# Optimization experiments

Measured on AMD Instinct MI355X. Metric: run time of the kernel, lower is better.

## Reference

```python
import jax, jax.numpy as jnp
import numpy as np

D_MODEL = 1024
D_MEMORY = 768
NUM_HEADS = 16
HEAD_DIM = D_MODEL // NUM_HEADS


def _linear_params(key, d_in, d_out):
    kw, kb = jax.random.split(key)
    bound = 1.0 / np.sqrt(d_in)
    W = jax.random.uniform(kw, (d_out, d_in), jnp.float32, -bound, bound)
    b = jax.random.uniform(kb, (d_out,), jnp.float32, -bound, bound)
    return W, b


def setup_inputs() -> dict:
    key = jax.random.key(0)
    ks = jax.random.split(key, 9)
    B, S, M = 2, 2048, 4096
    query = jax.random.normal(ks[0], (B, S, D_MODEL), jnp.float32)
    memory_keys = jax.random.normal(ks[1], (B, M, D_MEMORY), jnp.float32)
    memory_values = jax.random.normal(ks[2], (B, M, D_MEMORY), jnp.float32)
    Wq, bq = _linear_params(ks[3], D_MODEL, D_MODEL)
    Wk, bk = _linear_params(ks[4], D_MEMORY, D_MODEL)
    Wv, bv = _linear_params(ks[5], D_MEMORY, D_MODEL)
    Wo, bo = _linear_params(ks[6], D_MODEL, D_MODEL)
    Wg1, bg1 = _linear_params(ks[7], 2 * D_MODEL, D_MODEL)
    Wg2, bg2 = _linear_params(ks[8], D_MODEL, 1)
    return dict(query=query, memory_keys=memory_keys, memory_values=memory_values,
                Wq=Wq, bq=bq, Wk=Wk, bk=bk, Wv=Wv, bv=bv, Wo=Wo, bo=bo,
                Wg1=Wg1, bg1=bg1, Wg2=Wg2, bg2=bg2)


def reference(query, memory_keys, memory_values,
              Wq, bq, Wk, bk, Wv, bv, Wo, bo, Wg1, bg1, Wg2, bg2):
    B, S, _ = query.shape
    M = memory_keys.shape[1]
    H, Dh = NUM_HEADS, HEAD_DIM
    # projections (torch Linear: x @ W.T + b)
    Q = (query @ Wq.T + bq).reshape(B, S, H, Dh)
    K = (memory_keys @ Wk.T + bk).reshape(B, M, H, Dh)
    V = (memory_values @ Wv.T + bv).reshape(B, M, H, Dh)
    scale = Dh ** -0.5
    attn = jnp.einsum('bshd,bmhd->bhsm', Q, K) * scale
    attn = jax.nn.softmax(attn, axis=-1)
    retrieved = jnp.einsum('bhsm,bmhd->bshd', attn, V).reshape(B, S, H * Dh)
    retrieved = retrieved @ Wo.T + bo
    # gate: Linear -> SiLU -> Linear -> Sigmoid on [query; retrieved]
    g = jnp.concatenate([query, retrieved], axis=-1) @ Wg1.T + bg1
    g = jax.nn.silu(g)
    gate = jax.nn.sigmoid(g @ Wg2.T + bg2)  # [B,S,1]
    return query + gate * retrieved
```

## Files before the change

kernel.cpp:

```cpp
#include <hip/hip_runtime.h>

typedef __attribute__((ext_vector_type(8))) __bf16 bf16x8;
typedef __attribute__((ext_vector_type(4))) float f32x4;
typedef __attribute__((ext_vector_type(8))) unsigned short u16x8;

__device__ __forceinline__ ushort f2bf(float x) {
    unsigned u = __builtin_bit_cast(unsigned, x);
    unsigned r = u + 0x7fffu + ((u >> 16) & 1u);
    return (ushort)(r >> 16);
}
__device__ __forceinline__ float bf2f(ushort u) {
    unsigned v = ((unsigned)u) << 16;
    return __builtin_bit_cast(float, v);
}

__device__ __forceinline__ unsigned cvtpk(float lo, float hi) {
    unsigned r;
    asm("v_cvt_pk_bf16_f32 %0, %1, %2" : "=v"(r) : "v"(lo), "v"(hi));
    return r;
}

__device__ __forceinline__ void gload16(const void* g, void* l) {
    __builtin_amdgcn_global_load_lds(
        (const __attribute__((address_space(1))) void*)g,
        (__attribute__((address_space(3))) void*)l,
        16, 0, 0);
}

__global__ __launch_bounds__(256) void cvt_f32_bf16(const float* __restrict__ in,
                                                    ushort* __restrict__ out, int n4) {
    int i = blockIdx.x * 256 + threadIdx.x;
    int stride = gridDim.x * 256;
    for (; i < n4; i += stride) {
        float4 v = ((const float4*)in)[i];
        ushort4 o;
        o.x = f2bf(v.x); o.y = f2bf(v.y); o.z = f2bf(v.z); o.w = f2bf(v.w);
        ((ushort4*)out)[i] = o;
    }
}

__global__ __launch_bounds__(256) void cvt_query_cat(const float* __restrict__ in,
                                                     ushort* __restrict__ cat) {
    const int r = blockIdx.x, t = threadIdx.x;
    float4 v = ((const float4*)(in + (size_t)r * 1024))[t];
    ushort4 o;
    o.x = f2bf(v.x); o.y = f2bf(v.y); o.z = f2bf(v.z); o.w = f2bf(v.w);
    ((ushort4*)(cat + (size_t)r * 2048))[t] = o;
}

template<int EPI>
__global__ __launch_bounds__(256) void gemm_bt(
    const ushort* __restrict__ A, int lda,
    const ushort* __restrict__ Bw, int ldb,
    const float* __restrict__ bias,
    ushort* __restrict__ o_bf, int ld0,
    float* __restrict__ o_f32,
    int K, float scale)
{
    __shared__ __align__(1024) char smem[49152];
    char* As = smem;
    char* Bs = smem + 32768;
    const int t = threadIdx.x, w = t >> 6, l = t & 63, g = l >> 4, c = l & 15;
    const int wr = w >> 1, wc = w & 1;
    const long m0 = (long)blockIdx.y * 128, n0 = (long)blockIdx.x * 64;
    const size_t ldaB = (size_t)lda * 2, ldbB = (size_t)ldb * 2;
    const int swz = (c & 7) << 4;

    f32x4 acc[4][2];
#pragma unroll
    for (int i = 0; i < 4; ++i)
#pragma unroll
        for (int j = 0; j < 2; ++j) acc[i][j] = (f32x4)0.0f;

    auto stage = [&](int kt, int bufsel) {
        const char* Ab = (const char*)A + (size_t)kt * 128;
        const char* Bb = (const char*)Bw + (size_t)kt * 128;
#pragma unroll
        for (int i = 0; i < 4; ++i) {
            int o = (i * 4 + w) * 1024 + l * 16;
            int row = o >> 7, cb = o & 127;
            gload16(Ab + (size_t)(m0 + row) * ldaB + (cb ^ ((row & 7) << 4)),
                    As + bufsel * 16384 + (i * 4 + w) * 1024);
        }
#pragma unroll
        for (int i = 0; i < 2; ++i) {
            int o = (i * 4 + w) * 1024 + l * 16;
            int row = o >> 7, cb = o & 127;
            gload16(Bb + (size_t)(n0 + row) * ldbB + (cb ^ ((row & 7) << 4)),
                    Bs + bufsel * 8192 + (i * 4 + w) * 1024);
        }
    };

    const int nkt = K >> 6;
    stage(0, 0);
    __syncthreads();

    for (int kt = 0; kt < nkt; ++kt) {
        const int cur = kt & 1;
        if (kt + 1 < nkt) stage(kt + 1, cur ^ 1);
        const char* Ac = As + cur * 16384;
        const char* Bc = Bs + cur * 8192;
        bf16x8 af[2][4], bfr[2][2];
#pragma unroll
        for (int kf = 0; kf < 2; ++kf) {
            int cbk = (kf * 64 + g * 16) ^ swz;
#pragma unroll
            for (int i = 0; i < 4; ++i)
                af[kf][i] = *(const bf16x8*)(Ac + (wr * 64 + i * 16 + c) * 128 + cbk);
#pragma unroll
            for (int j = 0; j < 2; ++j)
                bfr[kf][j] = *(const bf16x8*)(Bc + (wc * 32 + j * 16 + c) * 128 + cbk);
        }
#pragma unroll
        for (int kf = 0; kf < 2; ++kf)
#pragma unroll
            for (int i = 0; i < 4; ++i)
#pragma unroll
                for (int j = 0; j < 2; ++j)
                    acc[i][j] = __builtin_amdgcn_mfma_f32_16x16x32_bf16(
                        af[kf][i], bfr[kf][j], acc[i][j], 0, 0, 0);
        __syncthreads();
    }

#pragma unroll
    for (int i = 0; i < 4; ++i)
#pragma unroll
        for (int j = 0; j < 2; ++j) {
            const long col = n0 + wc * 32 + j * 16 + c;
            const float bs = bias[col];
            const long rowb = m0 + wr * 64 + i * 16 + g * 4;
            if (EPI == 1) {
                ushort4 o;
                o.x = f2bf(acc[i][j][0] + bs);
                o.y = f2bf(acc[i][j][1] + bs);
                o.z = f2bf(acc[i][j][2] + bs);
                o.w = f2bf(acc[i][j][3] + bs);
                *(ushort4*)(o_bf + col * (long)ld0 + rowb) = o;
            } else {
#pragma unroll
                for (int jj = 0; jj < 4; ++jj) {
                    const long row = rowb + jj;
                    const float v = acc[i][j][jj] + bs;
                    if (EPI == 0) {
                        o_bf[row * (long)ld0 + col] = f2bf(v * scale);
                    } else if (EPI == 2) {
                        o_f32[row * (long)ld0 + col] = v;
                        o_bf[row * 2048 + col] = f2bf(v);
                    } else {
                        const float sv = v / (1.0f + __expf(-v));
                        o_bf[row * (long)ld0 + col] = f2bf(sv);
                    }
                }
            }
        }
}

__global__ __launch_bounds__(256, 4) void attn_fwd(
    const ushort* __restrict__ qp, const ushort* __restrict__ kp,
    const ushort* __restrict__ vT, ushort* __restrict__ out)
{
    __shared__ __align__(1024) char smem[40960];
    const int t = threadIdx.x, w = t >> 6, l = t & 63, g = l >> 4, c = l & 15;
    const int b = blockIdx.z, h = blockIdx.y;
    const int s0 = blockIdx.x * 64 + w * 16;
    const int swz = (c & 7) << 4;

    const size_t qbase = ((size_t)b * 2048 + s0 + c) * 1024 + h * 64 + g * 8;
    const bf16x8 qf0 = *(const bf16x8*)(qp + qbase);
    const bf16x8 qf1 = *(const bf16x8*)(qp + qbase + 32);

    const u16x8 ones_u = (u16x8)(ushort)0x3F80;
    const bf16x8 ones = __builtin_bit_cast(bf16x8, ones_u);

    f32x4 oacc[4];
    f32x4 lacc = (f32x4)0.0f;
#pragma unroll
    for (int d = 0; d < 4; ++d) oacc[d] = (f32x4)0.0f;
    float mrow = -1e30f;

    const char* kpB = (const char*)kp + (size_t)b * 4096 * 2048 + h * 128;
    const char* vTB = (const char*)vT + (size_t)h * 64 * 16384 + (size_t)b * 4096 * 2;
    char* Pw = smem + 32768 + w * 2048;

    auto stage = [&](int mt, int bufsel) {
#pragma unroll
        for (int i = 0; i < 2; ++i) {
            int o = (i * 4 + w) * 1024 + l * 16;
            int row = o >> 7, cb = o & 127;
            gload16(kpB + (size_t)(mt + row) * 2048 + (cb ^ ((row & 7) << 4)),
                    smem + bufsel * 8192 + (i * 4 + w) * 1024);
            gload16(vTB + (size_t)row * 16384 + (size_t)mt * 2 + (cb ^ ((row & 7) << 4)),
                    smem + 16384 + bufsel * 8192 + (i * 4 + w) * 1024);
        }
    };

    stage(0, 0);
    __syncthreads();

    for (int ti = 0; ti < 64; ++ti) {
        const int cur = ti & 1;
        if (ti < 63) stage((ti + 1) << 6, cur ^ 1);
        const char* Ksc = smem + cur * 8192;
        const char* Vsc = smem + 16384 + cur * 8192;

        f32x4 sacc[4];
#pragma unroll
        for (int mf = 0; mf < 4; ++mf) sacc[mf] = (f32x4)0.0f;
#pragma unroll
        for (int kf = 0; kf < 2; ++kf) {
            const int cbk = (kf * 64 + g * 16) ^ swz;
            const bf16x8 q = kf ? qf1 : qf0;
#pragma unroll
            for (int mf = 0; mf < 4; ++mf) {
                bf16x8 kb = *(const bf16x8*)(Ksc + (mf * 16 + c) * 128 + cbk);
                sacc[mf] = __builtin_amdgcn_mfma_f32_16x16x32_bf16(kb, q, sacc[mf], 0, 0, 0);
            }
        }

        float tm;
        {
            float a0 = fmaxf(fmaxf(sacc[0][0], sacc[0][1]), fmaxf(sacc[0][2], sacc[0][3]));
            float a1 = fmaxf(fmaxf(sacc[1][0], sacc[1][1]), fmaxf(sacc[1][2], sacc[1][3]));
            float a2 = fmaxf(fmaxf(sacc[2][0], sacc[2][1]), fmaxf(sacc[2][2], sacc[2][3]));
            float a3 = fmaxf(fmaxf(sacc[3][0], sacc[3][1]), fmaxf(sacc[3][2], sacc[3][3]));
            tm = fmaxf(fmaxf(a0, a1), fmaxf(a2, a3));
        }
        tm = fmaxf(tm, __shfl_xor(tm, 16));
        tm = fmaxf(tm, __shfl_xor(tm, 32));

        if (!__all(tm <= mrow + 8.0f)) {
            const float nm = fmaxf(mrow, tm);
            const float al = exp2f(mrow - nm);
            mrow = nm;
#pragma unroll
            for (int j = 0; j < 4; ++j) {
                const float alr = __shfl(al, g * 4 + j);
                lacc[j] *= alr;
#pragma unroll
                for (int df = 0; df < 4; ++df) oacc[df][j] *= alr;
            }
        }

        asm volatile("" ::: "memory");
#pragma unroll
        for (int mf = 0; mf < 4; ++mf) {
            const float p0 = exp2f(sacc[mf][0] - mrow);
            const float p1 = exp2f(sacc[mf][1] - mrow);
            const float p2 = exp2f(sacc[mf][2] - mrow);
            const float p3 = exp2f(sacc[mf][3] - mrow);
            const unsigned u0 = cvtpk(p0, p1);
            const unsigned u1 = cvtpk(p2, p3);
            const unsigned long long pw = ((unsigned long long)u1 << 32) | (unsigned long long)u0;
            *(unsigned long long*)(Pw + c * 128 + ((mf * 32 + g * 8) ^ swz)) = pw;
        }
        asm volatile("s_waitcnt lgkmcnt(0)" ::: "memory");
        __builtin_amdgcn_sched_barrier(0);
#pragma unroll
        for (int km = 0; km < 2; ++km) {
            const int cbm = (km * 64 + g * 16) ^ swz;
            const bf16x8 pa = *(const bf16x8*)(Pw + c * 128 + cbm);
            lacc = __builtin_amdgcn_mfma_f32_16x16x32_bf16(pa, ones, lacc, 0, 0, 0);
#pragma unroll
            for (int df = 0; df < 4; ++df) {
                bf16x8 vb = *(const bf16x8*)(Vsc + (df * 16 + c) * 128 + cbm);
                oacc[df] = __builtin_amdgcn_mfma_f32_16x16x32_bf16(pa, vb, oacc[df], 0, 0, 0);
            }
        }
        __builtin_amdgcn_sched_barrier(0);
        __syncthreads();
    }

    const size_t obase = ((size_t)b * 2048 + s0 + g * 4) * 1024 + h * 64 + c;
#pragma unroll
    for (int j = 0; j < 4; ++j) {
        const float rinv = 1.0f / lacc[j];
#pragma unroll
        for (int df = 0; df < 4; ++df)
            out[obase + (size_t)j * 1024 + df * 16] = f2bf(oacc[df][j] * rinv);
    }
}

__global__ __launch_bounds__(256) void gate_out_k(
    const ushort* __restrict__ gs, const float* __restrict__ Wg2,
    const float* __restrict__ bg2, const float* __restrict__ query,
    const float* __restrict__ retr, float* __restrict__ out)
{
    const int r = blockIdx.x, t = threadIdx.x, w = t >> 6, l = t & 63;
    ushort4 gv = ((const ushort4*)(gs + (size_t)r * 1024))[t];
    float4 wv = ((const float4*)Wg2)[t];
    float p = bf2f(gv.x) * wv.x + bf2f(gv.y) * wv.y + bf2f(gv.z) * wv.z + bf2f(gv.w) * wv.w;
    for (int m = 1; m < 64; m <<= 1) p += __shfl_xor(p, m);
    __shared__ float red[4];
    if (l == 0) red[w] = p;
    __syncthreads();
    const float dot = red[0] + red[1] + red[2] + red[3] + bg2[0];
    const float gate = 1.0f / (1.0f + __expf(-dot));
    float4 q = ((const float4*)(query + (size_t)r * 1024))[t];
    float4 rt = ((const float4*)(retr + (size_t)r * 1024))[t];
    float4 o;
    o.x = q.x + gate * rt.x; o.y = q.y + gate * rt.y;
    o.z = q.z + gate * rt.z; o.w = q.w + gate * rt.w;
    ((float4*)(out + (size_t)r * 1024))[t] = o;
}

extern "C" void kernel_launch(void* const* d_in, const int* in_sizes, int n_in,
                              void* d_out, int out_size, void* d_ws, size_t ws_size,
                              hipStream_t stream) {
    const float* query = (const float*)d_in[0];
    const float* mkeys = (const float*)d_in[1];
    const float* mvals = (const float*)d_in[2];
    const float* Wq  = (const float*)d_in[3];
    const float* bq  = (const float*)d_in[4];
    const float* Wk  = (const float*)d_in[5];
    const float* bk  = (const float*)d_in[6];
    const float* Wv  = (const float*)d_in[7];
    const float* bv  = (const float*)d_in[8];
    const float* Wo  = (const float*)d_in[9];
    const float* bo  = (const float*)d_in[10];
    const float* Wg1 = (const float*)d_in[11];
    const float* bg1 = (const float*)d_in[12];
    const float* Wg2 = (const float*)d_in[13];
    const float* bg2 = (const float*)d_in[14];
    float* outF = (float*)d_out;

    char* ws = (char*)d_ws;
    size_t off = 0;
    auto take = [&](size_t bytes) { char* p = ws + off; off += (bytes + 255) & ~(size_t)255; return p; };
    ushort* cat    = (ushort*)take((size_t)4096 * 2048 * 2);
    ushort* mkbf   = (ushort*)take((size_t)8192 * 768 * 2);
    ushort* mvbf   = (ushort*)take((size_t)8192 * 768 * 2);
    ushort* wqbf   = (ushort*)take((size_t)1024 * 1024 * 2);
    ushort* wkbf   = (ushort*)take((size_t)1024 * 768 * 2);
    ushort* wvbf   = (ushort*)take((size_t)1024 * 768 * 2);
    ushort* wobf   = (ushort*)take((size_t)1024 * 1024 * 2);
    ushort* wg1bf  = (ushort*)take((size_t)1024 * 2048 * 2);
    ushort* qproj  = (ushort*)take((size_t)4096 * 1024 * 2);
    ushort* kproj  = (ushort*)take((size_t)8192 * 1024 * 2);
    ushort* vprojT = (ushort*)take((size_t)1024 * 8192 * 2);
    ushort* attno  = (ushort*)take((size_t)4096 * 1024 * 2);
    float*  retro  = (float*)take((size_t)4096 * 1024 * 4);
    ushort* gsilu  = (ushort*)take((size_t)4096 * 1024 * 2);

    cvt_query_cat<<<4096, 256, 0, stream>>>(query, cat);
    cvt_f32_bf16<<<2048, 256, 0, stream>>>(mkeys, mkbf, 8192 * 768 / 4);
    cvt_f32_bf16<<<2048, 256, 0, stream>>>(mvals, mvbf, 8192 * 768 / 4);
    cvt_f32_bf16<<<512, 256, 0, stream>>>(Wq, wqbf, 1024 * 1024 / 4);
    cvt_f32_bf16<<<512, 256, 0, stream>>>(Wk, wkbf, 1024 * 768 / 4);
    cvt_f32_bf16<<<512, 256, 0, stream>>>(Wv, wvbf, 1024 * 768 / 4);
    cvt_f32_bf16<<<512, 256, 0, stream>>>(Wo, wobf, 1024 * 1024 / 4);
    cvt_f32_bf16<<<512, 256, 0, stream>>>(Wg1, wg1bf, 1024 * 2048 / 4);

    const float qscale = 0.125f * 1.44269504088896340736f;
    gemm_bt<0><<<dim3(16, 32), 256, 0, stream>>>(cat, 2048, wqbf, 1024, bq, qproj, 1024, nullptr, 1024, qscale);
    gemm_bt<0><<<dim3(16, 64), 256, 0, stream>>>(mkbf, 768, wkbf, 768, bk, kproj, 1024, nullptr, 768, 1.0f);
    gemm_bt<1><<<dim3(16, 64), 256, 0, stream>>>(mvbf, 768, wvbf, 768, bv, vprojT, 8192, nullptr, 768, 1.0f);
    attn_fwd<<<dim3(32, 16, 2), 256, 0, stream>>>(qproj, kproj, vprojT, attno);
    gemm_bt<2><<<dim3(16, 32), 256, 0, stream>>>(attno, 1024, wobf, 1024, bo, cat + 1024, 1024, retro, 1024, 1.0f);
    gemm_bt<3><<<dim3(16, 32), 256, 0, stream>>>(cat, 2048, wg1bf, 2048, bg1, gsilu, 1024, nullptr, 2048, 1.0f);
    gate_out_k<<<4096, 256, 0, stream>>>(gsilu, Wg2, bg2, query, retro, outF);
}
```

Baseline: 405.2 us.

## Merge conversion launches and hand-unroll GEMM and attention loops with precomputed addresses

Replaces seven separate f32-to-bf16 conversion launches with two merged kernels, one for memory keys/values and one for all five weights, to cut launch overhead. The GEMM and attention main loops are unrolled by two with compile-time buffer selection, and global source pointers and LDS read offsets are computed once and then incremented. The aim is less per-iteration address arithmetic and better instruction scheduling, at the cost of larger code and more live registers.

Measured after the change: 405.7 us. No clear change (+0.1%).

```diff
diff --git a/kernel.cpp b/kernel.cpp
--- a/kernel.cpp
+++ b/kernel.cpp
@@ -27,16 +27,42 @@
         16, 0, 0);
 }
 
-__global__ __launch_bounds__(256) void cvt_f32_bf16(const float* __restrict__ in,
-                                                    ushort* __restrict__ out, int n4) {
-    int i = blockIdx.x * 256 + threadIdx.x;
-    int stride = gridDim.x * 256;
-    for (; i < n4; i += stride) {
-        float4 v = ((const float4*)in)[i];
-        ushort4 o;
-        o.x = f2bf(v.x); o.y = f2bf(v.y); o.z = f2bf(v.z); o.w = f2bf(v.w);
-        ((ushort4*)out)[i] = o;
-    }
+#define MFMA16(a, b, cIn) __builtin_amdgcn_mfma_f32_16x16x32_bf16((a), (b), (cIn), 0, 0, 0)
+
+__global__ __launch_bounds__(256) void cvt_kv(const float* __restrict__ a, ushort* __restrict__ ab,
+                                              const float* __restrict__ bsrc, ushort* __restrict__ bb,
+                                              int n4) {
+    const int stride = gridDim.x * 256;
+    for (int i = blockIdx.x * 256 + threadIdx.x; i < n4; i += stride) {
+        float4 v = ((const float4*)a)[i];
+        ushort4 o; o.x = f2bf(v.x); o.y = f2bf(v.y); o.z = f2bf(v.z); o.w = f2bf(v.w);
+        ((ushort4*)ab)[i] = o;
+    }
+    for (int i = blockIdx.x * 256 + threadIdx.x; i < n4; i += stride) {
+        float4 v = ((const float4*)bsrc)[i];
+        ushort4 o; o.x = f2bf(v.x); o.y = f2bf(v.y); o.z = f2bf(v.z); o.w = f2bf(v.w);
+        ((ushort4*)bb)[i] = o;
+    }
+}
+
+__global__ __launch_bounds__(256) void cvt_weights(
+    const float* __restrict__ s0, ushort* __restrict__ d0, int n0,
+    const float* __restrict__ s1, ushort* __restrict__ d1, int n1,
+    const float* __restrict__ s2, ushort* __restrict__ d2, int n2,
+    const float* __restrict__ s3, ushort* __restrict__ d3, int n3,
+    const float* __restrict__ s4, ushort* __restrict__ d4, int n4c) {
+    const int stride = gridDim.x * 256;
+    const int t0 = blockIdx.x * 256 + threadIdx.x;
+#define CVT_SEG(S, D, N)                                                  \
+    for (int i = t0; i < (N); i += stride) {                              \
+        float4 v = ((const float4*)(S))[i];                               \
+        ushort4 o; o.x = f2bf(v.x); o.y = f2bf(v.y);                      \
+        o.z = f2bf(v.z); o.w = f2bf(v.w);                                 \
+        ((ushort4*)(D))[i] = o;                                           \
+    }
+    CVT_SEG(s0, d0, n0) CVT_SEG(s1, d1, n1) CVT_SEG(s2, d2, n2)
+    CVT_SEG(s3, d3, n3) CVT_SEG(s4, d4, n4c)
+#undef CVT_SEG
 }
 
 __global__ __launch_bounds__(256) void cvt_query_cat(const float* __restrict__ in,
@@ -58,13 +84,28 @@
     int K, float scale)
 {
     __shared__ __align__(1024) char smem[49152];
-    char* As = smem;
-    char* Bs = smem + 32768;
     const int t = threadIdx.x, w = t >> 6, l = t & 63, g = l >> 4, c = l & 15;
     const int wr = w >> 1, wc = w & 1;
     const long m0 = (long)blockIdx.y * 128, n0 = (long)blockIdx.x * 64;
     const size_t ldaB = (size_t)lda * 2, ldbB = (size_t)ldb * 2;
     const int swz = (c & 7) << 4;
+    const int o0 = w * 1024 + l * 16;
+
+    auto gsrc = [&](const char* base, size_t ldB, long r0, int o) {
+        const int row = o >> 7, cb = o & 127;
+        return base + (size_t)(r0 + row) * ldB + (cb ^ ((row & 7) << 4));
+    };
+    const char* aP0 = gsrc((const char*)A, ldaB, m0, o0);
+    const char* aP1 = gsrc((const char*)A, ldaB, m0, o0 + 4096);
+    const char* aP2 = gsrc((const char*)A, ldaB, m0, o0 + 8192);
+    const char* aP3 = gsrc((const char*)A, ldaB, m0, o0 + 12288);
+    const char* bP0 = gsrc((const char*)Bw, ldbB, n0, o0);
+    const char* bP1 = gsrc((const char*)Bw, ldbB, n0, o0 + 4096);
+
+    const int aRd0 = (wr * 64 + c) * 128 + ((g * 16) ^ swz);
+    const int aRd1 = aRd0 ^ 64;
+    const int bRd0 = 32768 + (wc * 32 + c) * 128 + ((g * 16) ^ swz);
+    const int bRd1 = bRd0 ^ 64;
 
     f32x4 acc[4][2];
 #pragma unroll
@@ -72,55 +113,54 @@
 #pragma unroll
         for (int j = 0; j < 2; ++j) acc[i][j] = (f32x4)0.0f;
 
-    auto stage = [&](int kt, int bufsel) {
-        const char* Ab = (const char*)A + (size_t)kt * 128;
-        const char* Bb = (const char*)Bw + (size_t)kt * 128;
-#pragma unroll
-        for (int i = 0; i < 4; ++i) {
-            int o = (i * 4 + w) * 1024 + l * 16;
-            int row = o >> 7, cb = o & 127;
-            gload16(Ab + (size_t)(m0 + row) * ldaB + (cb ^ ((row & 7) << 4)),
-                    As + bufsel * 16384 + (i * 4 + w) * 1024);
-        }
-#pragma unroll
-        for (int i = 0; i < 2; ++i) {
-            int o = (i * 4 + w) * 1024 + l * 16;
-            int row = o >> 7, cb = o & 127;
-            gload16(Bb + (size_t)(n0 + row) * ldbB + (cb ^ ((row & 7) << 4)),
-                    Bs + bufsel * 8192 + (i * 4 + w) * 1024);
-        }
-    };
+    gload16(aP0, smem + w * 1024);
+    gload16(aP1, smem + 4096 + w * 1024);
+    gload16(aP2, smem + 8192 + w * 1024);
+    gload16(aP3, smem + 12288 + w * 1024);
+    gload16(bP0, smem + 32768 + w * 1024);
+    gload16(bP1, smem + 32768 + 4096 + w * 1024);
+    aP0 += 128; aP1 += 128; aP2 += 128; aP3 += 128; bP0 += 128; bP1 += 128;
+    __syncthreads();
+
+#define GSTEP(CUR, PF)                                                          \
+    {                                                                           \
+        if (PF) {                                                               \
+            gload16(aP0, smem + ((CUR) ^ 1) * 16384 + w * 1024);                \
+            gload16(aP1, smem + ((CUR) ^ 1) * 16384 + 4096 + w * 1024);         \
+            gload16(aP2, smem + ((CUR) ^ 1) * 16384 + 8192 + w * 1024);         \
+            gload16(aP3, smem + ((CUR) ^ 1) * 16384 + 12288 + w * 1024);        \
+            gload16(bP0, smem + 32768 + ((CUR) ^ 1) * 8192 + w * 1024);         \
+            gload16(bP1, smem + 32768 + ((CUR) ^ 1) * 8192 + 4096 + w * 1024);  \
+            aP0 += 128; aP1 += 128; aP2 += 128; aP3 += 128;                     \
+            bP0 += 128; bP1 += 128;                                             \
+        }                                                                       \
+        _Pragma("unroll")                                                       \
+        for (int kf = 0; kf < 2; ++kf) {                                        \
+            const int ar = kf ? aRd1 : aRd0, br = kf ? bRd1 : bRd0;             \
+            bf16x8 af0 = *(const bf16x8*)(smem + (CUR) * 16384 + 0 + ar);       \
+            bf16x8 af1 = *(const bf16x8*)(smem + (CUR) * 16384 + 2048 + ar);    \
+            bf16x8 af2 = *(const bf16x8*)(smem + (CUR) * 16384 + 4096 + ar);    \
+            bf16x8 af3 = *(const bf16x8*)(smem + (CUR) * 16384 + 6144 + ar);    \
+            bf16x8 bf0 = *(const bf16x8*)(smem + (CUR) * 8192 + 0 + br);        \
+            bf16x8 bf1 = *(const bf16x8*)(smem + (CUR) * 8192 + 2048 + br);     \
+            acc[0][0] = MFMA16(af0, bf0, acc[0][0]);                            \
+            acc[0][1] = MFMA16(af0, bf1, acc[0][1]);                            \
+            acc[1][0] = MFMA16(af1, bf0, acc[1][0]);                            \
+            acc[1][1] = MFMA16(af1, bf1, acc[1][1]);                            \
+            acc[2][0] = MFMA16(af2, bf0, acc[2][0]);                            \
+            acc[2][1] = MFMA16(af2, bf1, acc[2][1]);                            \
+            acc[3][0] = MFMA16(af3, bf0, acc[3][0]);                            \
+            acc[3][1] = MFMA16(af3, bf1, acc[3][1]);                            \
+        }                                                                       \
+        __syncthreads();                                                        \
+    }
 
     const int nkt = K >> 6;
-    stage(0, 0);
-    __syncthreads();
-
-    for (int kt = 0; kt < nkt; ++kt) {
-        const int cur = kt & 1;
-        if (kt + 1 < nkt) stage(kt + 1, cur ^ 1);
-        const char* Ac = As + cur * 16384;
-        const char* Bc = Bs + cur * 8192;
-        bf16x8 af[2][4], bfr[2][2];
-#pragma unroll
-        for (int kf = 0; kf < 2; ++kf) {
-            int cbk = (kf * 64 + g * 16) ^ swz;
-#pragma unroll
-            for (int i = 0; i < 4; ++i)
-                af[kf][i] = *(const bf16x8*)(Ac + (wr * 64 + i * 16 + c) * 128 + cbk);
-#pragma unroll
-            for (int j = 0; j < 2; ++j)
-                bfr[kf][j] = *(const bf16x8*)(Bc + (wc * 32 + j * 16 + c) * 128 + cbk);
-        }
-#pragma unroll
-        for (int kf = 0; kf < 2; ++kf)
-#pragma unroll
-            for (int i = 0; i < 4; ++i)
-#pragma unroll
-                for (int j = 0; j < 2; ++j)
-                    acc[i][j] = __builtin_amdgcn_mfma_f32_16x16x32_bf16(
-                        af[kf][i], bfr[kf][j], acc[i][j], 0, 0, 0);
-        __syncthreads();
-    }
+    for (int kt = 0; kt < nkt; kt += 2) {
+        GSTEP(0, kt + 1 < nkt)
+        GSTEP(1, kt + 2 < nkt)
+    }
+#undef GSTEP
 
 #pragma unroll
     for (int i = 0; i < 4; ++i)
@@ -178,97 +218,132 @@
     for (int d = 0; d < 4; ++d) oacc[d] = (f32x4)0.0f;
     float mrow = -1e30f;
 
+    const int kb0 = c * 128 + ((g * 16) ^ swz);
+    const int kb1 = kb0 ^ 64;
+    const int pw0 = 32768 + w * 2048 + c * 128 + ((g * 8) ^ swz);
+    const int pwm1 = pw0 ^ 32, pwm2 = pw0 ^ 64, pwm3 = pw0 ^ 96;
+    const int pr0 = 32768 + w * 2048 + kb0;
+    const int pr1 = pr0 ^ 64;
+
     const char* kpB = (const char*)kp + (size_t)b * 4096 * 2048 + h * 128;
     const char* vTB = (const char*)vT + (size_t)h * 64 * 16384 + (size_t)b * 4096 * 2;
-    char* Pw = smem + 32768 + w * 2048;
-
-    auto stage = [&](int mt, int bufsel) {
-#pragma unroll
-        for (int i = 0; i < 2; ++i) {
-            int o = (i * 4 + w) * 1024 + l * 16;
-            int row = o >> 7, cb = o & 127;
-            gload16(kpB + (size_t)(mt + row) * 2048 + (cb ^ ((row & 7) << 4)),
-                    smem + bufsel * 8192 + (i * 4 + w) * 1024);
-            gload16(vTB + (size_t)row * 16384 + (size_t)mt * 2 + (cb ^ ((row & 7) << 4)),
-                    smem + 16384 + bufsel * 8192 + (i * 4 + w) * 1024);
-        }
+    const int o0 = w * 1024 + l * 16;
+    auto mksrc = [&](const char* base, size_t ldB, int o) {
+        const int row = o >> 7, cb = o & 127;
+        return base + (size_t)row * ldB + (cb ^ ((row & 7) << 4));
     };
-
-    stage(0, 0);
+    const char* kg0 = mksrc(kpB, 2048, o0);
+    const char* kg1 = mksrc(kpB, 2048, o0 + 4096);
+    const char* vg0 = mksrc(vTB, 16384, o0);
+    const char* vg1 = mksrc(vTB, 16384, o0 + 4096);
+
+    gload16(kg0, smem + w * 1024);
+    gload16(kg1, smem + 4096 + w * 1024);
+    gload16(vg0, smem + 16384 + w * 1024);
+    gload16(vg1, smem + 16384 + 4096 + w * 1024);
+    kg0 += 131072; kg1 += 131072; vg0 += 128; vg1 += 128;
     __syncthreads();
 
-    for (int ti = 0; ti < 64; ++ti) {
-        const int cur = ti & 1;
-        if (ti < 63) stage((ti + 1) << 6, cur ^ 1);
-        const char* Ksc = smem + cur * 8192;
-        const char* Vsc = smem + 16384 + cur * 8192;
-
-        f32x4 sacc[4];
-#pragma unroll
-        for (int mf = 0; mf < 4; ++mf) sacc[mf] = (f32x4)0.0f;
-#pragma unroll
-        for (int kf = 0; kf < 2; ++kf) {
-            const int cbk = (kf * 64 + g * 16) ^ swz;
-            const bf16x8 q = kf ? qf1 : qf0;
-#pragma unroll
-            for (int mf = 0; mf < 4; ++mf) {
-                bf16x8 kb = *(const bf16x8*)(Ksc + (mf * 16 + c) * 128 + cbk);
-                sacc[mf] = __builtin_amdgcn_mfma_f32_16x16x32_bf16(kb, q, sacc[mf], 0, 0, 0);
-            }
-        }
-
-        float tm;
-        {
-            float a0 = fmaxf(fmaxf(sacc[0][0], sacc[0][1]), fmaxf(sacc[0][2], sacc[0][3]));
-            float a1 = fmaxf(fmaxf(sacc[1][0], sacc[1][1]), fmaxf(sacc[1][2], sacc[1][3]));
-            float a2 = fmaxf(fmaxf(sacc[2][0], sacc[2][1]), fmaxf(sacc[2][2], sacc[2][3]));
-            float a3 = fmaxf(fmaxf(sacc[3][0], sacc[3][1]), fmaxf(sacc[3][2], sacc[3][3]));
-            tm = fmaxf(fmaxf(a0, a1), fmaxf(a2, a3));
-        }
-        tm = fmaxf(tm, __shfl_xor(tm, 16));
-        tm = fmaxf(tm, __shfl_xor(tm, 32));
-
-        if (!__all(tm <= mrow + 8.0f)) {
-            const float nm = fmaxf(mrow, tm);
-            const float al = exp2f(mrow - nm);
-            mrow = nm;
-#pragma unroll
-            for (int j = 0; j < 4; ++j) {
-                const float alr = __shfl(al, g * 4 + j);
-                lacc[j] *= alr;
-#pragma unroll
-                for (int df = 0; df < 4; ++df) oacc[df][j] *= alr;
-            }
-        }
-
-        asm volatile("" ::: "memory");
-#pragma unroll
-        for (int mf = 0; mf < 4; ++mf) {
-            const float p0 = exp2f(sacc[mf][0] - mrow);
-            const float p1 = exp2f(sacc[mf][1] - mrow);
-            const float p2 = exp2f(sacc[mf][2] - mrow);
-            const float p3 = exp2f(sacc[mf][3] - mrow);
-            const unsigned u0 = cvtpk(p0, p1);
-            const unsigned u1 = cvtpk(p2, p3);
-            const unsigned long long pw = ((unsigned long long)u1 << 32) | (unsigned long long)u0;
-            *(unsigned long long*)(Pw + c * 128 + ((mf * 32 + g * 8) ^ swz)) = pw;
-        }
-        asm volatile("s_waitcnt lgkmcnt(0)" ::: "memory");
-        __builtin_amdgcn_sched_barrier(0);
-#pragma unroll
-        for (int km = 0; km < 2; ++km) {
-            const int cbm = (km * 64 + g * 16) ^ swz;
-            const bf16x8 pa = *(const bf16x8*)(Pw + c * 128 + cbm);
-            lacc = __builtin_amdgcn_mfma_f32_16x16x32_bf16(pa, ones, lacc, 0, 0, 0);
-#pragma unroll
-            for (int df = 0; df < 4; ++df) {
-                bf16x8 vb = *(const bf16x8*)(Vsc + (df * 16 + c) * 128 + cbm);
-                oacc[df] = __builtin_amdgcn_mfma_f32_16x16x32_bf16(pa, vb, oacc[df], 0, 0, 0);
-            }
-        }
-        __builtin_amdgcn_sched_barrier(0);
-        __syncthreads();
-    }
+#define ATILE(CUR, PF)                                                          \
+    {                                                                           \
+        if (PF) {                                                               \
+            gload16(kg0, smem + ((CUR) ^ 1) * 8192 + w * 1024);                 \
+            gload16(kg1, smem + ((CUR) ^ 1) * 8192 + 4096 + w * 1024);          \
+            gload16(vg0, smem + 16384 + ((CUR) ^ 1) * 8192 + w * 1024);         \
+            gload16(vg1, smem + 16384 + ((CUR) ^ 1) * 8192 + 4096 + w * 1024);  \
+            kg0 += 131072; kg1 += 131072; vg0 += 128; vg1 += 128;               \
+        }                                                                       \
+        f32x4 s0v = (f32x4)0.0f, s1v = (f32x4)0.0f;                             \
+        f32x4 s2v = (f32x4)0.0f, s3v = (f32x4)0.0f;                             \
+        {                                                                       \
+            bf16x8 k0 = *(const bf16x8*)(smem + (CUR) * 8192 + 0 + kb0);        \
+            bf16x8 k1 = *(const bf16x8*)(smem + (CUR) * 8192 + 2048 + kb0);     \
+            bf16x8 k2 = *(const bf16x8*)(smem + (CUR) * 8192 + 4096 + kb0);     \
+            bf16x8 k3 = *(const bf16x8*)(smem + (CUR) * 8192 + 6144 + kb0);     \
+            s0v = MFMA16(k0, qf0, s0v); s1v = MFMA16(k1, qf0, s1v);             \
+            s2v = MFMA16(k2, qf0, s2v); s3v = MFMA16(k3, qf0, s3v);             \
+            k0 = *(const bf16x8*)(smem + (CUR) * 8192 + 0 + kb1);               \
+            k1 = *(const bf16x8*)(smem + (CUR) * 8192 + 2048 + kb1);            \
+            k2 = *(const bf16x8*)(smem + (CUR) * 8192 + 4096 + kb1);            \
+            k3 = *(const bf16x8*)(smem + (CUR) * 8192 + 6144 + kb1);            \
+            s0v = MFMA16(k0, qf1, s0v); s1v = MFMA16(k1, qf1, s1v);             \
+            s2v = MFMA16(k2, qf1, s2v); s3v = MFMA16(k3, qf1, s3v);             \
+        }                                                                       \
+        float tm;                                                               \
+        {                                                                       \
+            float a0 = fmaxf(fmaxf(s0v[0], s0v[1]), fmaxf(s0v[2], s0v[3]));     \
+            float a1 = fmaxf(fmaxf(s1v[0], s1v[1]), fmaxf(s1v[2], s1v[3]));     \
+            float a2 = fmaxf(fmaxf(s2v[0], s2v[1]), fmaxf(s2v[2], s2v[3]));     \
+            float a3 = fmaxf(fmaxf(s3v[0], s3v[1]), fmaxf(s3v[2], s3v[3]));     \
+            tm = fmaxf(fmaxf(a0, a1), fmaxf(a2, a3));                           \
+        }                                                                       \
+        tm = fmaxf(tm, __shfl_xor(tm, 16));                                     \
+        tm = fmaxf(tm, __shfl_xor(tm, 32));                                     \
+        if (!__all(tm <= mrow + 8.0f)) {                                        \
+            const float nm = fmaxf(mrow, tm);                                   \
+            const float al = exp2f(mrow - nm);                                  \
+            mrow = nm;                                                          \
+            _Pragma("unroll")                                                   \
+            for (int j = 0; j < 4; ++j) {                                       \
+                const float alr = __shfl(al, g * 4 + j);                        \
+                lacc[j] *= alr;                                                 \
+                oacc[0][j] *= alr; oacc[1][j] *= alr;                           \
+                oacc[2][j] *= alr; oacc[3][j] *= alr;                           \
+            }                                                                   \
+        }                                                                       \
+        asm volatile("" ::: "memory");                                          \
+        {                                                                       \
+            float p0 = exp2f(s0v[0] - mrow), p1 = exp2f(s0v[1] - mrow);         \
+            float p2 = exp2f(s0v[2] - mrow), p3 = exp2f(s0v[3] - mrow);         \
+            *(unsigned long long*)(smem + pw0) =                                \
+                ((unsigned long long)cvtpk(p2, p3) << 32) | cvtpk(p0, p1);      \
+            p0 = exp2f(s1v[0] - mrow); p1 = exp2f(s1v[1] - mrow);               \
+            p2 = exp2f(s1v[2] - mrow); p3 = exp2f(s1v[3] - mrow);               \
+            *(unsigned long long*)(smem + pwm1) =                               \
+                ((unsigned long long)cvtpk(p2, p3) << 32) | cvtpk(p0, p1);      \
+            p0 = exp2f(s2v[0] - mrow); p1 = exp2f(s2v[1] - mrow);               \
+            p2 = exp2f(s2v[2] - mrow); p3 = exp2f(s2v[3] - mrow);               \
+            *(unsigned long long*)(smem + pwm2) =                               \
+                ((unsigned long long)cvtpk(p2, p3) << 32) | cvtpk(p0, p1);      \
+            p0 = exp2f(s3v[0] - mrow); p1 = exp2f(s3v[1] - mrow);               \
+            p2 = exp2f(s3v[2] - mrow); p3 = exp2f(s3v[3] - mrow);               \
+            *(unsigned long long*)(smem + pwm3) =                               \
+                ((unsigned long long)cvtpk(p2, p3) << 32) | cvtpk(p0, p1);      \
+        }                                                                       \
+        asm volatile("s_waitcnt lgkmcnt(0)" ::: "memory");                      \
+        __builtin_amdgcn_sched_barrier(0);                                      \
+        {                                                                       \
+            bf16x8 pa = *(const bf16x8*)(smem + pr0);                           \
+            bf16x8 vb;                                                          \
+            lacc = MFMA16(pa, ones, lacc);                                      \
+            vb = *(const bf16x8*)(smem + 16384 + (CUR) * 8192 + 0 + kb0);       \
+            oacc[0] = MFMA16(pa, vb, oacc[0]);                                  \
+            vb = *(const bf16x8*)(smem + 16384 + (CUR) * 8192 + 2048 + kb0);    \
+            oacc[1] = MFMA16(pa, vb, oacc[1]);                                  \
+            vb = *(const bf16x8*)(smem + 16384 + (CUR) * 8192 + 4096 + kb0);    \
+            oacc[2] = MFMA16(pa, vb, oacc[2]);                                  \
+            vb = *(const bf16x8*)(smem + 16384 + (CUR) * 8192 + 6144 + kb0);    \
+            oacc[3] = MFMA16(pa, vb, oacc[3]);                                  \
+            pa = *(const bf16x8*)(smem + pr1);                                  \
+            lacc = MFMA16(pa, ones, lacc);                                      \
+            vb = *(const bf16x8*)(smem + 16384 + (CUR) * 8192 + 0 + kb1);       \
+            oacc[0] = MFMA16(pa, vb, oacc[0]);                                  \
+            vb = *(const bf16x8*)(smem + 16384 + (CUR) * 8192 + 2048 + kb1);    \
+            oacc[1] = MFMA16(pa, vb, oacc[1]);                                  \
+            vb = *(const bf16x8*)(smem + 16384 + (CUR) * 8192 + 4096 + kb1);    \
+            oacc[2] = MFMA16(pa, vb, oacc[2]);                                  \
+            vb = *(const bf16x8*)(smem + 16384 + (CUR) * 8192 + 6144 + kb1);    \
+            oacc[3] = MFMA16(pa, vb, oacc[3]);                                  \
+        }                                                                       \
+        __builtin_amdgcn_sched_barrier(0);                                      \
+        __syncthreads();                                                        \
+    }
+
+    for (int ti = 0; ti < 64; ti += 2) {
+        ATILE(0, true)
+        ATILE(1, ti < 62)
+    }
+#undef ATILE
 
     const size_t obase = ((size_t)b * 2048 + s0 + g * 4) * 1024 + h * 64 + c;
 #pragma unroll
@@ -342,13 +417,12 @@
     ushort* gsilu  = (ushort*)take((size_t)4096 * 1024 * 2);
 
     cvt_query_cat<<<4096, 256, 0, stream>>>(query, cat);
-    cvt_f32_bf16<<<2048, 256, 0, stream>>>(mkeys, mkbf, 8192 * 768 / 4);
-    cvt_f32_bf16<<<2048, 256, 0, stream>>>(mvals, mvbf, 8192 * 768 / 4);
-    cvt_f32_bf16<<<512, 256, 0, stream>>>(Wq, wqbf, 1024 * 1024 / 4);
-    cvt_f32_bf16<<<512, 256, 0, stream>>>(Wk, wkbf, 1024 * 768 / 4);
-    cvt_f32_bf16<<<512, 256, 0, stream>>>(Wv, wvbf, 1024 * 768 / 4);
-    cvt_f32_bf16<<<512, 256, 0, stream>>>(Wo, wobf, 1024 * 1024 / 4);
-    cvt_f32_bf16<<<512, 256, 0, stream>>>(Wg1, wg1bf, 1024 * 2048 / 4);
+    cvt_kv<<<2048, 256, 0, stream>>>(mkeys, mkbf, mvals, mvbf, 8192 * 768 / 4);
+    cvt_weights<<<1024, 256, 0, stream>>>(Wq, wqbf, 1024 * 1024 / 4,
+                                          Wk, wkbf, 1024 * 768 / 4,
+                                          Wv, wvbf, 1024 * 768 / 4,
+                                          Wo, wobf, 1024 * 1024 / 4,
+                                          Wg1, wg1bf, 1024 * 2048 / 4);
 
     const float qscale = 0.125f * 1.44269504088896340736f;
     gemm_bt<0><<<dim3(16, 32), 256, 0, stream>>>(cat, 2048, wqbf, 1024, bq, qproj, 1024, nullptr, 1024, qscale);
```
